# Kernel optimization log

Measured on AMD Instinct MI355X. Metric: run time of the kernel, lower is better.

## Reference

```python
import jax, jax.numpy as jnp
import numpy as np

N_HEADS = 6
N_POINTS = 4
EPS = 1e-6


def layer_norm(x, g, b):
    m = jnp.mean(x, axis=-1, keepdims=True)
    v = jnp.var(x, axis=-1, keepdims=True)
    return (x - m) * jax.lax.rsqrt(v + EPS) * g + b


def bilinear_sample(value_l, h, w, loc):
    """value_l: (B, h*w, H, Dh); loc: (B, Lq, H, P, 2) normalized to [0,1].
    grid_sample semantics: align_corners=False, padding_mode='zeros'.
    Returns (B, H, Lq, P, Dh)."""
    B, HW, Hh, Dh = value_l.shape
    Lq, P = loc.shape[1], loc.shape[3]
    v = jnp.transpose(value_l, (0, 2, 1, 3))  # (B,H,HW,Dh)
    x = loc[..., 0] * w - 0.5
    y = loc[..., 1] * h - 0.5
    x0 = jnp.floor(x)
    y0 = jnp.floor(y)
    wx = x - x0
    wy = y - y0

    def gather(xi, yi):
        valid = (xi >= 0) & (xi < w) & (yi >= 0) & (yi < h)
        xc = jnp.clip(xi, 0, w - 1).astype(jnp.int32)
        yc = jnp.clip(yi, 0, h - 1).astype(jnp.int32)
        idx = yc * w + xc  # (B,Lq,H,P)
        idx_t = jnp.transpose(idx, (0, 2, 1, 3)).reshape(B, Hh, Lq * P)
        g = jnp.take_along_axis(v, idx_t[..., None], axis=2)  # (B,H,Lq*P,Dh)
        g = g.reshape(B, Hh, Lq, P, Dh)
        m = jnp.transpose(valid, (0, 2, 1, 3))[..., None].astype(g.dtype)
        return g * m

    g00 = gather(x0, y0)
    g01 = gather(x0 + 1, y0)
    g10 = gather(x0, y0 + 1)
    g11 = gather(x0 + 1, y0 + 1)
    wx_t = jnp.transpose(wx, (0, 2, 1, 3))[..., None]
    wy_t = jnp.transpose(wy, (0, 2, 1, 3))[..., None]
    top = g00 * (1 - wx_t) + g01 * wx_t
    bot = g10 * (1 - wx_t) + g11 * wx_t
    return top * (1 - wy_t) + bot * wy_t


def ms_deform_attn(qn, ref, feat_n, Wv, bv, Woff, boff, Waw, baw, Wout, bout, shapes, starts):
    B, Lq, C = qn.shape
    Hh, P, Lv = N_HEADS, N_POINTS, len(shapes)
    Dh = C // Hh
    value = (feat_n @ Wv + bv).reshape(B, -1, Hh, Dh)
    off = (qn @ Woff + boff).reshape(B, Lq, Hh, Lv, P, 2)
    aw = (qn @ Waw + baw).reshape(B, Lq, Hh, Lv * P)
    aw = jax.nn.softmax(aw, axis=-1).reshape(B, Lq, Hh, Lv, P)
    # offset normalizer is [W, H] per level
    normalizer = jnp.asarray([[w_, h_] for (h_, w_) in shapes], dtype=qn.dtype)
    loc = ref[:, :, None, :, None, :] + off / normalizer[None, None, None, :, None, :]
    out = 0.0
    for l, (h_, w_) in enumerate(shapes):
        value_l = jax.lax.dynamic_slice_in_dim(value, starts[l], h_ * w_, axis=1)
        sampled = bilinear_sample(value_l, h_, w_, loc[:, :, :, l])  # (B,H,Lq,P,Dh)
        out = out + jnp.einsum('bhqpd,bqhp->bqhd', sampled, aw[:, :, :, l])
    out = out.reshape(B, Lq, C)
    return out @ Wout + bout


def setup_inputs() -> dict:
    key = jax.random.key(0)
    ks = jax.random.split(key, 12)
    B, Lq, C, M = 2, 4096, 384, 4
    H, P, Lv = N_HEADS, N_POINTS, 1
    s = 0.02
    inp = {}
    inp['query'] = jax.random.normal(ks[0], (B, Lq, C), jnp.float32)
    inp['reference_points'] = jax.random.uniform(ks[1], (B, Lq, Lv, 2), jnp.float32)
    inp['feat'] = jax.random.normal(ks[2], (B, Lq, C), jnp.float32)
    inp['feat_other'] = jax.random.normal(ks[3], (M - 1, B, Lq, C), jnp.float32)
    inp['qn_g'] = jnp.ones((C,), jnp.float32)
    inp['qn_b'] = jnp.zeros((C,), jnp.float32)
    inp['fn_g'] = jnp.ones((M, C), jnp.float32)
    inp['fn_b'] = jnp.zeros((M, C), jnp.float32)
    inp['Wv'] = jax.random.normal(ks[4], (M, C, C), jnp.float32) * s
    inp['bv'] = jnp.zeros((M, C), jnp.float32)
    inp['Woff'] = jax.random.normal(ks[5], (M, C, H * Lv * P * 2), jnp.float32) * s
    inp['boff'] = jax.random.normal(ks[6], (M, H * Lv * P * 2), jnp.float32) * 0.5
    inp['Waw'] = jax.random.normal(ks[7], (M, C, H * Lv * P), jnp.float32) * s
    inp['baw'] = jnp.zeros((M, H * Lv * P), jnp.float32)
    inp['Wout'] = jax.random.normal(ks[8], (M, C, C), jnp.float32) * s
    inp['bout'] = jnp.zeros((M, C), jnp.float32)
    inp['gamma'] = jax.random.normal(ks[9], (M, C), jnp.float32) * 0.1
    inp['spatial_shapes'] = np.array([[64, 64]], dtype=np.int64)
    inp['level_start_index'] = np.array([0], dtype=np.int64)
    return inp


def reference(query, reference_points, feat, feat_other, qn_g, qn_b, fn_g, fn_b,
              Wv, bv, Woff, boff, Waw, baw, Wout, bout, gamma,
              spatial_shapes, level_start_index):
    shapes = [(int(h), int(w)) for h, w in np.asarray(spatial_shapes)]
    starts = [int(v) for v in np.asarray(level_start_index)]
    qn = layer_norm(query, qn_g, qn_b)
    feats = [feat] + [feat_other[i] for i in range(feat_other.shape[0])]
    out = query
    for m in range(len(feats)):
        fn = layer_norm(feats[m], fn_g[m], fn_b[m])
        attn = ms_deform_attn(qn, reference_points, fn,
                              Wv[m], bv[m], Woff[m], boff[m],
                              Waw[m], baw[m], Wout[m], bout[m], shapes, starts)
        out = out + gamma[m] * attn
    return out
```

## Files before the change

kernel.cpp:

```cpp
#include <hip/hip_runtime.h>
#include <hip/hip_bf16.h>

#define RTOT 8192
#define C_   384
#define M_   4
#define KOUT 1536

typedef __bf16 bf16;
typedef bf16  bf16x8 __attribute__((ext_vector_type(8)));
typedef float f32x4  __attribute__((ext_vector_type(4)));

#define GLOAD_LDS16(g, l) __builtin_amdgcn_global_load_lds( \
    (const __attribute__((address_space(1))) unsigned int*)(g), \
    (__attribute__((address_space(3))) unsigned int*)(l), 16, 0, 0)

#define WAITB(N) do { \
    asm volatile("s_waitcnt vmcnt(" #N ")\n\ts_barrier" ::: "memory"); \
    __builtin_amdgcn_sched_barrier(0); } while (0)

#define S0 589824
#define S1 786432
#define S2 1376256
#define S3 1376768
#define S4 1377152

__global__ __launch_bounds__(256) void prep_kernel(
    const float* __restrict__ query, const float* __restrict__ feat,
    const float* __restrict__ feat_other,
    const float* __restrict__ qn_g, const float* __restrict__ qn_b,
    const float* __restrict__ fn_g, const float* __restrict__ fn_b,
    bf16* __restrict__ qn, bf16* __restrict__ fn,
    const float* __restrict__ Wv, const float* __restrict__ Woff,
    const float* __restrict__ Waw, const float* __restrict__ Wout,
    const float* __restrict__ gamma, const float* __restrict__ boff,
    const float* __restrict__ baw, const float* __restrict__ bout,
    bf16* __restrict__ WvT, bf16* __restrict__ WoffawT, bf16* __restrict__ WoutT,
    float* __restrict__ oabias, float* __restrict__ boutbig)
{
    const int bid = blockIdx.x;
    const int tid = threadIdx.x;
    if (bid < 10240) {
        const int which = bid / 2048;
        const int xb    = bid % 2048;
        const int r = xb * 4 + (tid >> 6);
        const int lane = tid & 63;
        const float* src; const float* g; const float* bb; bf16* dst;
        if (which == 0) { src = query; g = qn_g; bb = qn_b; dst = qn; }
        else {
            int m = which - 1;
            src = (m == 0) ? feat : feat_other + (size_t)(m - 1) * RTOT * C_;
            g = fn_g + m * C_; bb = fn_b + m * C_; dst = fn + (size_t)m * RTOT * C_;
        }
        src += (size_t)r * C_; dst += (size_t)r * C_;
        float2 v[3]; float s = 0.f, sq = 0.f;
#pragma unroll
        for (int j = 0; j < 3; ++j) {
            v[j] = *reinterpret_cast<const float2*>(src + (lane + j * 64) * 2);
            s += v[j].x + v[j].y; sq += v[j].x * v[j].x + v[j].y * v[j].y;
        }
#pragma unroll
        for (int o = 1; o < 64; o <<= 1) {
            s += __shfl_xor(s, o);
            sq += __shfl_xor(sq, o);
        }
        const float mean = s * (1.f / C_);
        const float var  = sq * (1.f / C_) - mean * mean;
        const float rs   = rsqrtf(var + 1e-6f);
#pragma unroll
        for (int j = 0; j < 3; ++j) {
            const int c = (lane + j * 64) * 2;
            union { bf16 h2[2]; unsigned int u; } o;
            o.h2[0] = (bf16)((v[j].x - mean) * rs * g[c] + bb[c]);
            o.h2[1] = (bf16)((v[j].y - mean) * rs * g[c + 1] + bb[c + 1]);
            *reinterpret_cast<unsigned int*>(dst + c) = o.u;
        }
        return;
    }
    for (int idx = (bid - 10240) * 256 + tid; idx < S4; idx += 1024 * 256) {
        if (idx < S0) {
            int t = idx; int m = t / (C_ * C_); int rr = t % (C_ * C_);
            int n = rr / C_, k = rr % C_;
            WvT[t] = (bf16)Wv[(size_t)m * C_ * C_ + (size_t)k * C_ + n];
        } else if (idx < S1) {
            int t = idx - S0; int m = t / (128 * C_); int rr = t % (128 * C_);
            int n = rr / C_, k = rr % C_;
            float v = 0.f;
            if (n < 48)      v = Woff[(size_t)m * C_ * 48 + (size_t)k * 48 + n];
            else if (n < 72) v = Waw[(size_t)m * C_ * 24 + (size_t)k * 24 + (n - 48)];
            WoffawT[t] = (bf16)v;
        } else if (idx < S2) {
            int t = idx - S1; int n = t / KOUT; int kk = t % KOUT;
            int m = kk / C_, k = kk % C_;
            WoutT[t] = (bf16)(Wout[(size_t)m * C_ * C_ + (size_t)k * C_ + n] * gamma[m * C_ + n]);
        } else if (idx < S3) {
            int t = idx - S2; int m = t / 128; int n = t % 128;
            float v = 0.f;
            if (n < 48)      v = boff[m * 48 + n];
            else if (n < 72) v = baw[m * 24 + (n - 48)];
            oabias[t] = v;
        } else {
            int c = idx - S3;
            float s = 0.f;
            for (int m = 0; m < M_; ++m) s += gamma[m * C_ + c] * bout[m * C_ + c];
            boutbig[c] = s;
        }
    }
}

__device__ __forceinline__ void gemm_pipe(
    const bf16* __restrict__ A, int lda,
    const bf16* __restrict__ W, int ldw,
    const float* __restrict__ bias,
    void* __restrict__ outP, int ldo, int mode,
    int brow, int bcol, bf16* As, bf16* Bs)
{
    const int tid = threadIdx.x;
    const int lane = tid & 63, wave = tid >> 6;
    const int wr = wave >> 1, wc = wave & 1;
    const int lr = lane & 15, lg = lane >> 4;

    const int r0 = tid >> 2, s0 = tid & 3;
    const int r1 = r0 + 64;
    const long long aoff0 = (long long)(brow + r0) * lda + (s0 ^ ((r0 >> 1) & 3)) * 8;
    const long long aoff1 = (long long)(brow + r1) * lda + (s0 ^ ((r1 >> 1) & 3)) * 8;
    const long long woff0 = (long long)(bcol + r0) * ldw + (s0 ^ ((r0 >> 1) & 3)) * 8;
    const long long woff1 = (long long)(bcol + r1) * ldw + (s0 ^ ((r1 >> 1) & 3)) * 8;

    int aRd[4], bRd[4];
#pragma unroll
    for (int i = 0; i < 4; ++i) {
        const int ra = wr * 64 + i * 16 + lr;
        const int rb = wc * 64 + i * 16 + lr;
        aRd[i] = ra * 32 + (lg ^ ((ra >> 1) & 3)) * 8;
        bRd[i] = rb * 32 + (lg ^ ((rb >> 1) & 3)) * 8;
    }

    f32x4 acc[4][4] = {};

#pragma unroll
    for (int t = 0; t < 2; ++t) {
        GLOAD_LDS16(A + aoff0 + t * 32, (char*)As + t * 8192 + tid * 16);
        GLOAD_LDS16(A + aoff1 + t * 32, (char*)As + t * 8192 + (tid + 256) * 16);
        GLOAD_LDS16(W + woff0 + t * 32, (char*)Bs + t * 8192 + tid * 16);
        GLOAD_LDS16(W + woff1 + t * 32, (char*)Bs + t * 8192 + (tid + 256) * 16);
    }

#pragma unroll
    for (int kt = 0; kt < 12; ++kt) {
        if (kt + 1 < 12) { WAITB(4); } else { WAITB(0); }
        const int cb = kt % 3, ib = (kt + 2) % 3;
        if (kt + 2 < 12) {
            GLOAD_LDS16(A + aoff0 + (kt + 2) * 32, (char*)As + ib * 8192 + tid * 16);
            GLOAD_LDS16(A + aoff1 + (kt + 2) * 32, (char*)As + ib * 8192 + (tid + 256) * 16);
            GLOAD_LDS16(W + woff0 + (kt + 2) * 32, (char*)Bs + ib * 8192 + tid * 16);
            GLOAD_LDS16(W + woff1 + (kt + 2) * 32, (char*)Bs + ib * 8192 + (tid + 256) * 16);
        }
        bf16x8 af[4], bfr[4];
#pragma unroll
        for (int mi = 0; mi < 4; ++mi)
            af[mi] = *reinterpret_cast<const bf16x8*>(&As[cb * 4096 + aRd[mi]]);
#pragma unroll
        for (int ni = 0; ni < 4; ++ni)
            bfr[ni] = *reinterpret_cast<const bf16x8*>(&Bs[cb * 4096 + bRd[ni]]);
#pragma unroll
        for (int mi = 0; mi < 4; ++mi)
#pragma unroll
            for (int ni = 0; ni < 4; ++ni)
                acc[mi][ni] = __builtin_amdgcn_mfma_f32_16x16x32_bf16(
                    af[mi], bfr[ni], acc[mi][ni], 0, 0, 0);
    }

#pragma unroll
    for (int mi = 0; mi < 4; ++mi) {
#pragma unroll
        for (int ni = 0; ni < 4; ++ni) {
#pragma unroll
            for (int rr = 0; rr < 4; ++rr) {
                const int row = brow + wr * 64 + mi * 16 + lg * 4 + rr;
                const int col = bcol + wc * 64 + ni * 16 + lr;
                float v = acc[mi][ni][rr];
                if (mode != 3) v += bias[col];
                const long long o = (long long)row * ldo + col;
                if (mode == 1) ((float*)outP)[o] = v;
                else           ((bf16*)outP)[o] = (bf16)v;
            }
        }
    }
}

__global__ __launch_bounds__(256) void g01_kernel(
    const bf16* __restrict__ fn, const bf16* __restrict__ qn,
    const bf16* __restrict__ WvT, const bf16* __restrict__ WoffawT,
    const float* __restrict__ bv, const float* __restrict__ oabias,
    bf16* __restrict__ value, float* __restrict__ offaw)
{
    __shared__ __align__(16) bf16 As[3 * 4096];
    __shared__ __align__(16) bf16 Bs[3 * 4096];
    const int id = blockIdx.x;
    if (id < 768) {
        const int rowb = id & 63, q = id >> 6;
        const int colb = q % 3, m = q / 3;
        gemm_pipe(fn + (long long)m * RTOT * C_, C_,
                  WvT + (long long)m * C_ * C_, C_,
                  bv + m * C_, value + (long long)m * RTOT * C_, C_, 0,
                  rowb * 128, colb * 128, As, Bs);
    } else {
        const int id2 = id - 768;
        const int rowb = id2 & 63, m = id2 >> 6;
        gemm_pipe(qn, C_, WoffawT + (long long)m * 128 * C_, C_,
                  oabias + m * 128, offaw + (long long)m * RTOT * 128, 128, 1,
                  rowb * 128, 0, As, Bs);
    }
}

__global__ __launch_bounds__(256) void g2_kernel(
    const bf16* __restrict__ attn, const bf16* __restrict__ WoutT,
    bf16* __restrict__ partial)
{
    __shared__ __align__(16) bf16 As[3 * 4096];
    __shared__ __align__(16) bf16 Bs[3 * 4096];
    const int rowb = blockIdx.x & 63;
    const int q = blockIdx.x >> 6;
    const int colb = q % 3, kc = q / 3;
    gemm_pipe(attn + kc * C_, KOUT, WoutT + kc * C_, KOUT, nullptr,
              partial + (long long)kc * RTOT * C_, C_, 3,
              rowb * 128, colb * 128, As, Bs);
}

__global__ __launch_bounds__(256) void combine_kernel(
    const bf16* __restrict__ partial, const float* __restrict__ query,
    const float* __restrict__ boutbig, float* __restrict__ out)
{
    const int i8 = (blockIdx.x * 256 + threadIdx.x) * 8;
    const int c0 = i8 % C_;
    float s[8];
#pragma unroll
    for (int j = 0; j < 8; ++j) s[j] = query[i8 + j] + boutbig[c0 + j];
#pragma unroll
    for (int z = 0; z < 4; ++z) {
        bf16x8 p = *reinterpret_cast<const bf16x8*>(partial + (long long)z * RTOT * C_ + i8);
#pragma unroll
        for (int j = 0; j < 8; ++j) s[j] += (float)p[j];
    }
#pragma unroll
    for (int j = 0; j < 8; ++j) out[i8 + j] = s[j];
}

struct WP { float w; int off; };

__global__ __launch_bounds__(384) void sample_kernel(
    const float* __restrict__ offaw, const float* __restrict__ ref,
    const bf16* __restrict__ value, bf16* __restrict__ attn)
{
    const int bid   = blockIdx.x;
    const int combo = bid & 7;
    const int quad  = bid >> 3;
    const int m = combo >> 1, b = combo & 1;
    const int r0 = b * 4096 + quad * 4;

    __shared__ WP wp_s[4][24][4];

    const int t = threadIdx.x;
    if (t < 96) {
        const int row = t / 24;
        const int i   = t % 24;
        const int h = i >> 2, p = i & 3;
        const int r = r0 + row;
        const float* oa = offaw + ((long long)m * RTOT + r) * 128;
        float e = oa[48 + h * 4 + p];
        float mx = fmaxf(e, __shfl_xor(e, 1));
        mx = fmaxf(mx, __shfl_xor(mx, 2));
        float ex = expf(e - mx);
        float s = ex;
        s += __shfl_xor(s, 1);
        s += __shfl_xor(s, 2);
        const float aw = ex / s;
        const float x = ref[r * 2 + 0] * 64.f - 0.5f + oa[h * 8 + p * 2 + 0];
        const float y = ref[r * 2 + 1] * 64.f - 0.5f + oa[h * 8 + p * 2 + 1];
        const float xf = floorf(x), yf = floorf(y);
        const float wx = x - xf, wy = y - yf;
        const int x0 = (int)xf, y0 = (int)yf;
        const bool xok0 = (x0 >= 0) && (x0 < 64);
        const bool xok1 = (x0 >= -1) && (x0 < 63);
        const bool yok0 = (y0 >= 0) && (y0 < 64);
        const bool yok1 = (y0 >= -1) && (y0 < 63);
        const int xc0 = min(max(x0, 0), 63),     xc1 = min(max(x0 + 1, 0), 63);
        const int yc0 = min(max(y0, 0), 63),     yc1 = min(max(y0 + 1, 0), 63);
        WP w0 = { aw * (1.f - wx) * (1.f - wy) * (float)(xok0 && yok0), (yc0 * 64 + xc0) * (C_ * 2) };
        WP w1 = { aw * wx         * (1.f - wy) * (float)(xok1 && yok0), (yc0 * 64 + xc1) * (C_ * 2) };
        WP w2 = { aw * (1.f - wx) * wy         * (float)(xok0 && yok1), (yc1 * 64 + xc0) * (C_ * 2) };
        WP w3 = { aw * wx         * wy         * (float)(xok1 && yok1), (yc1 * 64 + xc1) * (C_ * 2) };
        wp_s[row][i][0] = w0;  wp_s[row][i][1] = w1;
        wp_s[row][i][2] = w2;  wp_s[row][i][3] = w3;
    }
    __syncthreads();

    const int row = t / 96;
    const int tl  = t % 96;
    const int h   = tl >> 4;
    const int l16 = tl & 15;
    const int r   = r0 + row;
    const char* vb = (const char*)(value
        + ((long long)m * RTOT + (long long)b * 4096) * C_ + h * 64 + l16 * 4);

    float wreg[16]; int oreg[16]; unsigned long long vreg[16];
#pragma unroll
    for (int i = 0; i < 16; ++i) {
        WP wp = wp_s[row][h * 4 + (i >> 2)][i & 3];
        wreg[i] = wp.w; oreg[i] = wp.off;
    }
#pragma unroll
    for (int i = 0; i < 16; ++i)
        vreg[i] = *reinterpret_cast<const unsigned long long*>(vb + oreg[i]);
    float a0 = 0.f, a1 = 0.f, a2 = 0.f, a3 = 0.f;
#pragma unroll
    for (int i = 0; i < 16; ++i) {
        const unsigned int lo = (unsigned int)vreg[i];
        const unsigned int hi = (unsigned int)(vreg[i] >> 32);
        a0 += wreg[i] * __builtin_bit_cast(float, lo << 16);
        a1 += wreg[i] * __builtin_bit_cast(float, lo & 0xffff0000u);
        a2 += wreg[i] * __builtin_bit_cast(float, hi << 16);
        a3 += wreg[i] * __builtin_bit_cast(float, hi & 0xffff0000u);
    }
    union { bf16 h4[4]; unsigned long long u; } o;
    o.h4[0] = (bf16)a0; o.h4[1] = (bf16)a1; o.h4[2] = (bf16)a2; o.h4[3] = (bf16)a3;
    *reinterpret_cast<unsigned long long*>(attn + (long long)r * KOUT + m * C_ + h * 64 + l16 * 4) = o.u;
}

extern "C" void kernel_launch(void* const* d_in, const int* in_sizes, int n_in,
                              void* d_out, int out_size, void* d_ws, size_t ws_size,
                              hipStream_t stream)
{
    const float* query      = (const float*)d_in[0];
    const float* ref        = (const float*)d_in[1];
    const float* feat       = (const float*)d_in[2];
    const float* feat_other = (const float*)d_in[3];
    const float* qn_g = (const float*)d_in[4];
    const float* qn_b = (const float*)d_in[5];
    const float* fn_g = (const float*)d_in[6];
    const float* fn_b = (const float*)d_in[7];
    const float* Wv   = (const float*)d_in[8];
    const float* bv   = (const float*)d_in[9];
    const float* Woff = (const float*)d_in[10];
    const float* boff = (const float*)d_in[11];
    const float* Waw  = (const float*)d_in[12];
    const float* baw  = (const float*)d_in[13];
    const float* Wout = (const float*)d_in[14];
    const float* bout = (const float*)d_in[15];
    const float* gamma = (const float*)d_in[16];
    float* out = (float*)d_out;

    char* ws = (char*)d_ws;
    size_t off = 0;
    auto carve = [&](size_t bytes) { char* p = ws + off; off += (bytes + 255) & ~(size_t)255; return p; };
    bf16*  qn      = (bf16*)carve((size_t)RTOT * C_ * 2);
    bf16*  fn      = (bf16*)carve((size_t)M_ * RTOT * C_ * 2);
    bf16*  value   = (bf16*)carve((size_t)M_ * RTOT * C_ * 2);
    bf16*  attn    = (bf16*)carve((size_t)RTOT * KOUT * 2);
    bf16*  partial = (bf16*)carve((size_t)M_ * RTOT * C_ * 2);
    float* offaw   = (float*)carve((size_t)M_ * RTOT * 128 * 4);
    bf16*  WvT     = (bf16*)carve((size_t)M_ * C_ * C_ * 2);
    bf16*  WoffawT = (bf16*)carve((size_t)M_ * 128 * C_ * 2);
    bf16*  WoutT   = (bf16*)carve((size_t)C_ * KOUT * 2);
    float* oabias  = (float*)carve((size_t)M_ * 128 * 4);
    float* boutbig = (float*)carve((size_t)C_ * 4);

    prep_kernel<<<11264, 256, 0, stream>>>(query, feat, feat_other,
                                           qn_g, qn_b, fn_g, fn_b, qn, fn,
                                           Wv, Woff, Waw, Wout, gamma, boff, baw, bout,
                                           WvT, WoffawT, WoutT, oabias, boutbig);
    g01_kernel<<<1024, 256, 0, stream>>>(fn, qn, WvT, WoffawT, bv, oabias, value, offaw);
    sample_kernel<<<dim3(RTOT * M_ / 4), 384, 0, stream>>>(offaw, ref, value, attn);
    g2_kernel<<<768, 256, 0, stream>>>(attn, WoutT, partial);
    combine_kernel<<<1536, 256, 0, stream>>>(partial, query, boutbig, out);
}
```

Measured before the change: 107.3 us.

## Fuse split-K output GEMM with combine into single full-K deep-pipelined kernel

Replaces the split-K output projection (bf16 partials per model) plus a separate combine kernel with one GEMM over the full K=1536 that adds bias and the residual query in its epilogue. It uses an 8-stage LDS ring with async global-to-LDS loads. This removes the partial-buffer write/read traffic and a kernel launch. It risks underfilling the GPU, since only 192 blocks with large LDS footprints run at one block per CU.

```diff
diff --git a/kernel.cpp b/kernel.cpp
--- a/kernel.cpp
+++ b/kernel.cpp
@@ -178,8 +178,7 @@
             for (int rr = 0; rr < 4; ++rr) {
                 const int row = brow + wr * 64 + mi * 16 + lg * 4 + rr;
                 const int col = bcol + wc * 64 + ni * 16 + lr;
-                float v = acc[mi][ni][rr];
-                if (mode != 3) v += bias[col];
+                float v = acc[mi][ni][rr] + bias[col];
                 const long long o = (long long)row * ldo + col;
                 if (mode == 1) ((float*)outP)[o] = v;
                 else           ((bf16*)outP)[o] = (bf16)v;
@@ -215,35 +214,88 @@
 
 __global__ __launch_bounds__(256) void g2_kernel(
     const bf16* __restrict__ attn, const bf16* __restrict__ WoutT,
-    bf16* __restrict__ partial)
-{
-    __shared__ __align__(16) bf16 As[3 * 4096];
-    __shared__ __align__(16) bf16 Bs[3 * 4096];
-    const int rowb = blockIdx.x & 63;
-    const int q = blockIdx.x >> 6;
-    const int colb = q % 3, kc = q / 3;
-    gemm_pipe(attn + kc * C_, KOUT, WoutT + kc * C_, KOUT, nullptr,
-              partial + (long long)kc * RTOT * C_, C_, 3,
-              rowb * 128, colb * 128, As, Bs);
-}
-
-__global__ __launch_bounds__(256) void combine_kernel(
-    const bf16* __restrict__ partial, const float* __restrict__ query,
-    const float* __restrict__ boutbig, float* __restrict__ out)
-{
-    const int i8 = (blockIdx.x * 256 + threadIdx.x) * 8;
-    const int c0 = i8 % C_;
-    float s[8];
-#pragma unroll
-    for (int j = 0; j < 8; ++j) s[j] = query[i8 + j] + boutbig[c0 + j];
-#pragma unroll
-    for (int z = 0; z < 4; ++z) {
-        bf16x8 p = *reinterpret_cast<const bf16x8*>(partial + (long long)z * RTOT * C_ + i8);
-#pragma unroll
-        for (int j = 0; j < 8; ++j) s[j] += (float)p[j];
-    }
-#pragma unroll
-    for (int j = 0; j < 8; ++j) out[i8 + j] = s[j];
+    const float* __restrict__ query, const float* __restrict__ boutbig,
+    float* __restrict__ out)
+{
+    __shared__ __align__(16) bf16 As[8 * 4096];
+    __shared__ __align__(16) bf16 Bs[8 * 4096];
+    const int brow = (blockIdx.x & 63) * 128;
+    const int bcol = (blockIdx.x >> 6) * 128;
+    const int tid = threadIdx.x;
+    const int lane = tid & 63, wave = tid >> 6;
+    const int wr = wave >> 1, wc = wave & 1;
+    const int lr = lane & 15, lg = lane >> 4;
+
+    const int r0 = tid >> 2, s0 = tid & 3;
+    const int r1 = r0 + 64;
+    const long long aoff0 = (long long)(brow + r0) * KOUT + (s0 ^ ((r0 >> 1) & 3)) * 8;
+    const long long aoff1 = (long long)(brow + r1) * KOUT + (s0 ^ ((r1 >> 1) & 3)) * 8;
+    const long long woff0 = (long long)(bcol + r0) * KOUT + (s0 ^ ((r0 >> 1) & 3)) * 8;
+    const long long woff1 = (long long)(bcol + r1) * KOUT + (s0 ^ ((r1 >> 1) & 3)) * 8;
+
+    int aRd[4], bRd[4];
+#pragma unroll
+    for (int i = 0; i < 4; ++i) {
+        const int ra = wr * 64 + i * 16 + lr;
+        const int rb = wc * 64 + i * 16 + lr;
+        aRd[i] = ra * 32 + (lg ^ ((ra >> 1) & 3)) * 8;
+        bRd[i] = rb * 32 + (lg ^ ((rb >> 1) & 3)) * 8;
+    }
+
+#pragma unroll
+    for (int t = 0; t < 7; ++t) {
+        GLOAD_LDS16(attn + aoff0 + t * 32, (char*)As + t * 8192 + tid * 16);
+        GLOAD_LDS16(attn + aoff1 + t * 32, (char*)As + t * 8192 + (tid + 256) * 16);
+        GLOAD_LDS16(WoutT + woff0 + t * 32, (char*)Bs + t * 8192 + tid * 16);
+        GLOAD_LDS16(WoutT + woff1 + t * 32, (char*)Bs + t * 8192 + (tid + 256) * 16);
+    }
+
+    f32x4 acc[4][4] = {};
+#pragma unroll
+    for (int kt = 0; kt < 48; ++kt) {
+        if (kt <= 41)      { WAITB(24); }
+        else if (kt == 42) { WAITB(20); }
+        else if (kt == 43) { WAITB(16); }
+        else if (kt == 44) { WAITB(12); }
+        else if (kt == 45) { WAITB(8);  }
+        else if (kt == 46) { WAITB(4);  }
+        else               { WAITB(0);  }
+        if (kt + 7 < 48) {
+            const int ib = (kt + 7) & 7;
+            GLOAD_LDS16(attn + aoff0 + (kt + 7) * 32, (char*)As + ib * 8192 + tid * 16);
+            GLOAD_LDS16(attn + aoff1 + (kt + 7) * 32, (char*)As + ib * 8192 + (tid + 256) * 16);
+            GLOAD_LDS16(WoutT + woff0 + (kt + 7) * 32, (char*)Bs + ib * 8192 + tid * 16);
+            GLOAD_LDS16(WoutT + woff1 + (kt + 7) * 32, (char*)Bs + ib * 8192 + (tid + 256) * 16);
+        }
+        const int cb = kt & 7;
+        bf16x8 af[4], bfr[4];
+#pragma unroll
+        for (int mi = 0; mi < 4; ++mi)
+            af[mi] = *reinterpret_cast<const bf16x8*>(&As[cb * 4096 + aRd[mi]]);
+#pragma unroll
+        for (int ni = 0; ni < 4; ++ni)
+            bfr[ni] = *reinterpret_cast<const bf16x8*>(&Bs[cb * 4096 + bRd[ni]]);
+#pragma unroll
+        for (int mi = 0; mi < 4; ++mi)
+#pragma unroll
+            for (int ni = 0; ni < 4; ++ni)
+                acc[mi][ni] = __builtin_amdgcn_mfma_f32_16x16x32_bf16(
+                    af[mi], bfr[ni], acc[mi][ni], 0, 0, 0);
+    }
+
+#pragma unroll
+    for (int mi = 0; mi < 4; ++mi) {
+#pragma unroll
+        for (int ni = 0; ni < 4; ++ni) {
+#pragma unroll
+            for (int rr = 0; rr < 4; ++rr) {
+                const int row = brow + wr * 64 + mi * 16 + lg * 4 + rr;
+                const int col = bcol + wc * 64 + ni * 16 + lr;
+                const long long o = (long long)row * C_ + col;
+                out[o] = acc[mi][ni][rr] + boutbig[col] + query[o];
+            }
+        }
+    }
 }
 
 struct WP { float w; int off; };
@@ -357,7 +409,6 @@
     bf16*  fn      = (bf16*)carve((size_t)M_ * RTOT * C_ * 2);
     bf16*  value   = (bf16*)carve((size_t)M_ * RTOT * C_ * 2);
     bf16*  attn    = (bf16*)carve((size_t)RTOT * KOUT * 2);
-    bf16*  partial = (bf16*)carve((size_t)M_ * RTOT * C_ * 2);
     float* offaw   = (float*)carve((size_t)M_ * RTOT * 128 * 4);
     bf16*  WvT     = (bf16*)carve((size_t)M_ * C_ * C_ * 2);
     bf16*  WoffawT = (bf16*)carve((size_t)M_ * 128 * C_ * 2);
@@ -371,6 +422,5 @@
                                            WvT, WoffawT, WoutT, oabias, boutbig);
     g01_kernel<<<1024, 256, 0, stream>>>(fn, qn, WvT, WoffawT, bv, oabias, value, offaw);
     sample_kernel<<<dim3(RTOT * M_ / 4), 384, 0, stream>>>(offaw, ref, value, attn);
-    g2_kernel<<<768, 256, 0, stream>>>(attn, WoutT, partial);
-    combine_kernel<<<1536, 256, 0, stream>>>(partial, query, boutbig, out);
-}
+    g2_kernel<<<192, 256, 0, stream>>>(attn, WoutT, query, boutbig, out);
+}
```

New measurement: 104.2 us. 1.03x faster.
